# Performance work log

Measured on AMD Instinct MI355X. Metric: run time of the kernel, lower is better.

## Reference

```python
import jax, jax.numpy as jnp
import numpy as np

N, E, D, H, B = 10000, 160000, 128, 1, 4
SLOPE = 0.01  # negative_slope from DeepQNet default


def gat_layer(x, node_state, src, dst, W, att_src, att_dst, Wns, bns, bias):
    # x: [N,D] or [B,N,D]; node_state: [B,N,1]
    xs = x + node_state @ Wns + bns              # [B,N,D]
    Bx, Nn = xs.shape[0], xs.shape[1]
    h = (xs @ W).reshape(Bx, Nn, H, D)           # [B,N,H,C]
    a_src = (h * att_src).sum(-1)                # [B,N,H]
    a_dst = (h * att_dst).sum(-1)                # [B,N,H]
    ae = a_src[:, src] + a_dst[:, dst]           # [B,Etot,H]
    ae = jnp.where(ae > 0, ae, SLOPE * ae)       # leaky_relu
    ae_t = jnp.moveaxis(ae, 1, 0)                # [Etot,B,H]
    m = jax.ops.segment_max(ae_t, dst, num_segments=Nn)   # [N,B,H]
    e = jnp.exp(ae_t - m[dst])
    s = jax.ops.segment_sum(e, dst, num_segments=Nn)
    alpha = e / s[dst]                           # [Etot,B,H]
    h_e = jnp.moveaxis(h, 1, 0)                  # [N,B,H,C]
    msg = alpha[..., None] * h_e[src]            # [Etot,B,H,C]
    out = jax.ops.segment_sum(msg, dst, num_segments=Nn)  # [N,B,H,C]
    out = jnp.moveaxis(out, 0, 1).mean(2) + bias # concat=False -> head mean
    return jax.nn.relu(out)


def setup_inputs() -> dict:
    key = jax.random.key(0)
    ks = jax.random.split(key, 16)
    edges = jax.random.randint(ks[0], (2, E), 0, N)
    loop = jnp.arange(N)
    edge_index = jnp.concatenate([edges, jnp.stack([loop, loop])], axis=1)  # add_self_loops
    state = jax.random.uniform(ks[1], (B, N), dtype=jnp.float32)
    strucEmb = jax.random.normal(ks[2], (N, D), dtype=jnp.float32) * 0.1
    s = 0.05
    return {
        "state": state,
        "strucEmb": strucEmb,
        "edge_index": edge_index,
        "gat_W": jax.random.normal(ks[3], (3, D, H * D), dtype=jnp.float32) * s,
        "gat_att_src": jax.random.normal(ks[4], (3, H, D), dtype=jnp.float32) * s,
        "gat_att_dst": jax.random.normal(ks[5], (3, H, D), dtype=jnp.float32) * s,
        "gat_Wns": jax.random.normal(ks[6], (3, 1, D), dtype=jnp.float32) * s,
        "gat_bns": jnp.zeros((3, D), jnp.float32),
        "gat_bias": jnp.zeros((3, D), jnp.float32),
        "W1": jax.random.normal(ks[7], (D, D), dtype=jnp.float32) * s,
        "b1": jnp.zeros((D,), jnp.float32),
        "W2": jax.random.normal(ks[8], (D, D), dtype=jnp.float32) * s,
        "b2": jnp.zeros((D,), jnp.float32),
        "W3": jax.random.normal(ks[9], (2 * D, 1), dtype=jnp.float32) * s,
        "b3": jnp.zeros((1,), jnp.float32),
    }


def reference(state, strucEmb, edge_index, gat_W, gat_att_src, gat_att_dst,
              gat_Wns, gat_bns, gat_bias, W1, b1, W2, b2, W3, b3):
    src, dst = edge_index[0], edge_index[1]
    rs = state.reshape(state.shape[0], N, 1)     # [B,N,1]
    x = strucEmb
    for l in range(3):
        x = gat_layer(x, rs, src, dst, gat_W[l], gat_att_src[l], gat_att_dst[l],
                      gat_Wns[l], gat_bns[l], gat_bias[l])
    state_emb = x.sum(1)                         # [B,D]
    beta_state = state_emb @ W1 + b1             # [B,D]
    beta_action = x @ W2 + b2                    # [B,N,D]  (is_for_learn=True path)
    expand_state = jnp.broadcast_to(beta_state[:, None, :], beta_action.shape)
    out = jax.nn.relu(jnp.concatenate([expand_state, beta_action], axis=2))
    return out @ W3 + b3                         # [B,N,1]
```

## Files before the change

kernel.cpp:

```cpp
#include <hip/hip_runtime.h>
#include <math.h>

#define N_NODES 10000
#define B_SZ 4
#define SLOPE 0.01f
#define BN (B_SZ * N_NODES)
#define PADK 136

typedef __attribute__((ext_vector_type(8))) short short8;
typedef __attribute__((ext_vector_type(4))) short short4v;
typedef __attribute__((ext_vector_type(4))) float float4v;

__device__ __forceinline__ unsigned short f2bf(float f) {
    unsigned u = __builtin_bit_cast(unsigned, f);
    u += 0x7fffu + ((u >> 16) & 1u);
    return (unsigned short)(u >> 16);
}
__device__ __forceinline__ float bf2f(unsigned short s) {
    unsigned u = ((unsigned)s) << 16;
    return __builtin_bit_cast(float, u);
}


__global__ __launch_bounds__(256) void init_kernel(int* deg, int* cursor, float* state_emb) {
    int i = blockIdx.x * 256 + threadIdx.x;
    if (i < N_NODES) { deg[i] = 0; cursor[i] = 0; }
    if (i < B_SZ * 128) state_emb[i] = 0.f;
}

__global__ __launch_bounds__(256) void hist_kernel(const int* __restrict__ dst, int Etot, int* deg) {
    int e = blockIdx.x * 256 + threadIdx.x;
    if (e < Etot) atomicAdd(&deg[dst[e]], 1);
}

__global__ __launch_bounds__(1024) void scan_kernel(const int* __restrict__ deg, int* __restrict__ rowOff) {
    __shared__ int wsum[16];
    int tid = threadIdx.x;
    int lane = tid & 63, wid = tid >> 6;
    int base = tid * 10;
    int v[10]; int tot = 0;
#pragma unroll
    for (int j = 0; j < 10; j++) {
        int idx = base + j;
        int d = (idx < N_NODES) ? deg[idx] : 0;
        tot += d; v[j] = tot;
    }
    int incl = tot;
    for (int off = 1; off < 64; off <<= 1) {
        int t = __shfl_up(incl, off, 64);
        if (lane >= off) incl += t;
    }
    if (lane == 63) wsum[wid] = incl;
    __syncthreads();
    if (wid == 0) {
        int wv = (lane < 16) ? wsum[lane] : 0;
        for (int off = 1; off < 16; off <<= 1) {
            int t = __shfl_up(wv, off, 64);
            if (lane >= off) wv += t;
        }
        if (lane < 16) wsum[lane] = wv;
    }
    __syncthreads();
    int waveoff = (wid > 0) ? wsum[wid - 1] : 0;
    int excl = waveoff + incl - tot;
    if (tid == 0) rowOff[0] = 0;
#pragma unroll
    for (int j = 0; j < 10; j++) {
        int idx = base + j;
        if (idx < N_NODES) rowOff[idx + 1] = excl + v[j];
    }
}

__global__ __launch_bounds__(256) void scatter_kernel(const int* __restrict__ dst, int Etot,
                                                      const int* __restrict__ rowOff,
                                                      int* cursor, int* __restrict__ edgeLst) {
    int e = blockIdx.x * 256 + threadIdx.x;
    if (e < Etot) {
        int d = dst[e];
        int pos = rowOff[d] + atomicAdd(&cursor[d], 1);
        edgeLst[pos] = e;
    }
}


__global__ __launch_bounds__(256) void wconv_kernel(const float* __restrict__ gatW,
                                                    const float* __restrict__ W2,
                                                    unsigned short* __restrict__ whi,
                                                    unsigned short* __restrict__ wlo) {
    int w = blockIdx.y;
    int i = blockIdx.x * 256 + threadIdx.x;
    int k = i >> 7, c = i & 127;
    const float* src = (w < 3) ? (gatW + (size_t)w * 16384) : W2;
    float v = src[k * 128 + c];
    unsigned short h = f2bf(v);
    whi[w * 16384 + c * 128 + k] = h;
    wlo[w * 16384 + c * 128 + k] = f2bf(v - bf2f(h));
}


__global__ __launch_bounds__(256) void gemm_att_mfma(
    const float* __restrict__ xin, int layer0,
    const float* __restrict__ state,
    const unsigned short* __restrict__ WThi, const unsigned short* __restrict__ WTlo,
    const float* __restrict__ attS, const float* __restrict__ attD,
    const float* __restrict__ Wns, const float* __restrict__ bns,
    unsigned short* __restrict__ Hout, float* __restrict__ aSrcP, float* __restrict__ aDstP)
{
    __shared__ __align__(16) char smem[64 * PADK * 2 * 2];
    unsigned short* sAh = (unsigned short*)smem;
    unsigned short* sAl = sAh + 64 * PADK;
    unsigned short* sCus = (unsigned short*)smem;
    __shared__ float sWns[128], sBns[128], sAs[128], sAd[128];
    __shared__ float sPart[64 * 4 * 2];

    int tid = threadIdx.x;
    int g0 = blockIdx.x * 64;
    int w = tid >> 6, lane = tid & 63;
    int quad = lane >> 4, mcol = lane & 15;

    if (tid < 128) {
        sWns[tid] = Wns[tid]; sBns[tid] = bns[tid];
        sAs[tid] = attS[tid]; sAd[tid] = attD[tid];
    }

    short8 Bh[4][2], Bl[4][2];
#pragma unroll
    for (int kc = 0; kc < 4; kc++)
#pragma unroll
        for (int nt = 0; nt < 2; nt++) {
            int col = w * 32 + nt * 16 + mcol;
            Bh[kc][nt] = *(const short8*)(WThi + col * 128 + kc * 32 + quad * 8);
            Bl[kc][nt] = *(const short8*)(WTlo + col * 128 + kc * 32 + quad * 8);
        }

    __syncthreads();

    for (int i4 = tid; i4 < 64 * 32; i4 += 256) {
        int r = i4 >> 5, k4 = (i4 & 31) << 2;
        int g = g0 + r, n = g >> 2, b = g & 3;
        const float* src = layer0 ? (xin + (size_t)n * 128 + k4) : (xin + (size_t)g * 128 + k4);
        float4 v = *(const float4*)src;
        float st = state[b * N_NODES + n];
        float x0 = v.x + st * sWns[k4]     + sBns[k4];
        float x1 = v.y + st * sWns[k4 + 1] + sBns[k4 + 1];
        float x2 = v.z + st * sWns[k4 + 2] + sBns[k4 + 2];
        float x3 = v.w + st * sWns[k4 + 3] + sBns[k4 + 3];
        unsigned short h0 = f2bf(x0), h1 = f2bf(x1), h2 = f2bf(x2), h3 = f2bf(x3);
        short4v hv = { (short)h0, (short)h1, (short)h2, (short)h3 };
        short4v lv = { (short)f2bf(x0 - bf2f(h0)), (short)f2bf(x1 - bf2f(h1)),
                       (short)f2bf(x2 - bf2f(h2)), (short)f2bf(x3 - bf2f(h3)) };
        *(short4v*)(sAh + r * PADK + k4) = hv;
        *(short4v*)(sAl + r * PADK + k4) = lv;
    }
    __syncthreads();

    float4v acc[4][2];
#pragma unroll
    for (int mt = 0; mt < 4; mt++)
#pragma unroll
        for (int nt = 0; nt < 2; nt++) acc[mt][nt] = (float4v){0.f, 0.f, 0.f, 0.f};

#pragma unroll
    for (int kc = 0; kc < 4; kc++) {
#pragma unroll
        for (int mt = 0; mt < 4; mt++) {
            short8 ah = *(const short8*)(sAh + (mt * 16 + mcol) * PADK + kc * 32 + quad * 8);
            short8 al = *(const short8*)(sAl + (mt * 16 + mcol) * PADK + kc * 32 + quad * 8);
#pragma unroll
            for (int nt = 0; nt < 2; nt++) {
                acc[mt][nt] = __builtin_amdgcn_mfma_f32_16x16x32_bf16(ah, Bh[kc][nt], acc[mt][nt], 0, 0, 0);
                acc[mt][nt] = __builtin_amdgcn_mfma_f32_16x16x32_bf16(al, Bh[kc][nt], acc[mt][nt], 0, 0, 0);
                acc[mt][nt] = __builtin_amdgcn_mfma_f32_16x16x32_bf16(ah, Bl[kc][nt], acc[mt][nt], 0, 0, 0);
            }
        }
    }

    __syncthreads();

    float pp[16], pd[16];
#pragma unroll
    for (int r16 = 0; r16 < 16; r16++) { pp[r16] = 0.f; pd[r16] = 0.f; }
#pragma unroll
    for (int mt = 0; mt < 4; mt++)
#pragma unroll
        for (int nt = 0; nt < 2; nt++)
#pragma unroll
            for (int reg = 0; reg < 4; reg++) {
                int row = mt * 16 + quad * 4 + reg;
                int col = w * 32 + nt * 16 + mcol;
                float v = acc[mt][nt][reg];
                sCus[row * PADK + col] = f2bf(v);
                pp[mt * 4 + reg] += v * sAs[col];
                pd[mt * 4 + reg] += v * sAd[col];
            }
#pragma unroll
    for (int off = 1; off < 16; off <<= 1)
#pragma unroll
        for (int r16 = 0; r16 < 16; r16++) {
            pp[r16] += __shfl_xor(pp[r16], off);
            pd[r16] += __shfl_xor(pd[r16], off);
        }
    if (mcol == 0) {
#pragma unroll
        for (int r16 = 0; r16 < 16; r16++) {
            int row = (r16 >> 2) * 16 + quad * 4 + (r16 & 3);
            sPart[row * 8 + w * 2 + 0] = pp[r16];
            sPart[row * 8 + w * 2 + 1] = pd[r16];
        }
    }
    __syncthreads();

    for (int i = tid; i < 64 * 16; i += 256) {
        int r = i >> 4, c8 = i & 15;
        uint4 u = *(uint4*)(sCus + r * PADK + c8 * 8);
        *(uint4*)(Hout + (size_t)(g0 + r) * 128 + c8 * 8) = u;
    }
    if (tid < 64) {
        float s0 = sPart[tid * 8] + sPart[tid * 8 + 2] + sPart[tid * 8 + 4] + sPart[tid * 8 + 6];
        float s1 = sPart[tid * 8 + 1] + sPart[tid * 8 + 3] + sPart[tid * 8 + 5] + sPart[tid * 8 + 7];
        aSrcP[g0 + tid] = s0;
        aDstP[g0 + tid] = s1;
    }
}


__global__ __launch_bounds__(256) void sm_agg_kernel(
    const int* __restrict__ rowOff, const int* __restrict__ edgeLst,
    const int* __restrict__ srcArr,
    const float* __restrict__ aSrcP, const float* __restrict__ aDstP,
    const unsigned short* __restrict__ H,
    const float* __restrict__ bias, float* __restrict__ Xout)
{
    __shared__ int sSrc[64];
    __shared__ float sAl[64 * 4];
    int n = blockIdx.x;
    int start = rowOff[n], end = rowOff[n + 1];
    int tid = threadIdx.x;
    int b = tid >> 6, t = tid & 63;
    float adst = aDstP[n * 4 + b];

    float m = -1e30f;
    for (int i = start + t; i < end; i += 64) {
        int sn = srcArr[edgeLst[i]];
        float v = aSrcP[sn * 4 + b] + adst;
        m = fmaxf(m, v > 0.f ? v : SLOPE * v);
    }
    m = fmaxf(m, __shfl_xor(m, 1));  m = fmaxf(m, __shfl_xor(m, 2));
    m = fmaxf(m, __shfl_xor(m, 4));  m = fmaxf(m, __shfl_xor(m, 8));
    m = fmaxf(m, __shfl_xor(m, 16)); m = fmaxf(m, __shfl_xor(m, 32));

    float s = 0.f;
    for (int i = start + t; i < end; i += 64) {
        int sn = srcArr[edgeLst[i]];
        float v = aSrcP[sn * 4 + b] + adst;
        float ae = v > 0.f ? v : SLOPE * v;
        s += __expf(ae - m);
    }
    s += __shfl_xor(s, 1);  s += __shfl_xor(s, 2);  s += __shfl_xor(s, 4);
    s += __shfl_xor(s, 8);  s += __shfl_xor(s, 16); s += __shfl_xor(s, 32);
    float inv = 1.f / s;

    float accx = 0.f, accy = 0.f;
    const unsigned int* Hu = (const unsigned int*)H;
    for (int c0 = start; c0 < end; c0 += 64) {
        int cnt = min(64, end - c0);
        if (t < cnt) {
            int e = edgeLst[c0 + t];
            int sn = srcArr[e];
            if (b == 0) sSrc[t] = sn;
            float v = aSrcP[sn * 4 + b] + adst;
            float ae = v > 0.f ? v : SLOPE * v;
            sAl[t * 4 + b] = __expf(ae - m) * inv;
        }
        __syncthreads();
        int j = 0;
        for (; j + 4 <= cnt; j += 4) {
            int s0 = sSrc[j], s1 = sSrc[j + 1], s2 = sSrc[j + 2], s3 = sSrc[j + 3];
            float a0 = sAl[j * 4 + b], a1 = sAl[(j + 1) * 4 + b];
            float a2 = sAl[(j + 2) * 4 + b], a3 = sAl[(j + 3) * 4 + b];
            unsigned int h0 = Hu[(size_t)(s0 * 4 + b) * 64 + t];
            unsigned int h1 = Hu[(size_t)(s1 * 4 + b) * 64 + t];
            unsigned int h2 = Hu[(size_t)(s2 * 4 + b) * 64 + t];
            unsigned int h3 = Hu[(size_t)(s3 * 4 + b) * 64 + t];
            accx += a0 * __builtin_bit_cast(float, h0 << 16) + a1 * __builtin_bit_cast(float, h1 << 16)
                  + a2 * __builtin_bit_cast(float, h2 << 16) + a3 * __builtin_bit_cast(float, h3 << 16);
            accy += a0 * __builtin_bit_cast(float, h0 & 0xffff0000u) + a1 * __builtin_bit_cast(float, h1 & 0xffff0000u)
                  + a2 * __builtin_bit_cast(float, h2 & 0xffff0000u) + a3 * __builtin_bit_cast(float, h3 & 0xffff0000u);
        }
        for (; j < cnt; j++) {
            int s0 = sSrc[j];
            float a0 = sAl[j * 4 + b];
            unsigned int h0 = Hu[(size_t)(s0 * 4 + b) * 64 + t];
            accx += a0 * __builtin_bit_cast(float, h0 << 16);
            accy += a0 * __builtin_bit_cast(float, h0 & 0xffff0000u);
        }
        __syncthreads();
    }
    float ox = accx + bias[2 * t];
    float oy = accy + bias[2 * t + 1];
    ((float2*)Xout)[(size_t)(n * 4 + b) * 64 + t] = make_float2(ox > 0.f ? ox : 0.f, oy > 0.f ? oy : 0.f);
}


__global__ __launch_bounds__(128) void sum_nodes_kernel(const float* __restrict__ X, float* state_emb) {
    int cx = blockIdx.x, b = blockIdx.y, d = threadIdx.x;
    int n0 = cx * 157, n1 = n0 + 157;
    if (n1 > N_NODES) n1 = N_NODES;
    float acc = 0.f;
    for (int n = n0; n < n1; n++) acc += X[(size_t)(n * 4 + b) * 128 + d];
    atomicAdd(&state_emb[b * 128 + d], acc);
}

__global__ __launch_bounds__(512) void beta_state_kernel(
    const float* __restrict__ state_emb, const float* __restrict__ W1,
    const float* __restrict__ b1, const float* __restrict__ W3, float* c1)
{
    __shared__ float sm[512];
    int tid = threadIdx.x;
    int b = tid >> 7, d = tid & 127;
    float acc = b1[d];
    for (int k = 0; k < 128; k++) acc += state_emb[b * 128 + k] * W1[k * 128 + d];
    float v = acc > 0.f ? acc : 0.f;
    sm[tid] = v * W3[d];
    __syncthreads();
    for (int s = 64; s > 0; s >>= 1) {
        if (d < s) sm[tid] += sm[tid + s];
        __syncthreads();
    }
    if (d == 0) c1[b] = sm[tid];
}


__global__ __launch_bounds__(256) void final_mfma(
    const float* __restrict__ X,
    const unsigned short* __restrict__ WThi, const unsigned short* __restrict__ WTlo,
    const float* __restrict__ b2, const float* __restrict__ W3,
    const float* __restrict__ b3, const float* __restrict__ c1,
    float* __restrict__ out)
{
    __shared__ __align__(16) char smem[64 * PADK * 2 * 2];
    unsigned short* sAh = (unsigned short*)smem;
    unsigned short* sAl = sAh + 64 * PADK;
    __shared__ float sB2[128], sW3[128];
    __shared__ float sPart[64 * 4];

    int tid = threadIdx.x;
    int g0 = blockIdx.x * 64;
    int w = tid >> 6, lane = tid & 63;
    int quad = lane >> 4, mcol = lane & 15;

    if (tid < 128) { sB2[tid] = b2[tid]; sW3[tid] = W3[128 + tid]; }

    short8 Bh[4][2], Bl[4][2];
#pragma unroll
    for (int kc = 0; kc < 4; kc++)
#pragma unroll
        for (int nt = 0; nt < 2; nt++) {
            int col = w * 32 + nt * 16 + mcol;
            Bh[kc][nt] = *(const short8*)(WThi + col * 128 + kc * 32 + quad * 8);
            Bl[kc][nt] = *(const short8*)(WTlo + col * 128 + kc * 32 + quad * 8);
        }

    for (int i4 = tid; i4 < 64 * 32; i4 += 256) {
        int r = i4 >> 5, k4 = (i4 & 31) << 2;
        int g = g0 + r;
        float4 v = *(const float4*)(X + (size_t)g * 128 + k4);
        unsigned short h0 = f2bf(v.x), h1 = f2bf(v.y), h2 = f2bf(v.z), h3 = f2bf(v.w);
        short4v hv = { (short)h0, (short)h1, (short)h2, (short)h3 };
        short4v lv = { (short)f2bf(v.x - bf2f(h0)), (short)f2bf(v.y - bf2f(h1)),
                       (short)f2bf(v.z - bf2f(h2)), (short)f2bf(v.w - bf2f(h3)) };
        *(short4v*)(sAh + r * PADK + k4) = hv;
        *(short4v*)(sAl + r * PADK + k4) = lv;
    }
    __syncthreads();

    float4v acc[4][2];
#pragma unroll
    for (int mt = 0; mt < 4; mt++)
#pragma unroll
        for (int nt = 0; nt < 2; nt++) acc[mt][nt] = (float4v){0.f, 0.f, 0.f, 0.f};

#pragma unroll
    for (int kc = 0; kc < 4; kc++) {
#pragma unroll
        for (int mt = 0; mt < 4; mt++) {
            short8 ah = *(const short8*)(sAh + (mt * 16 + mcol) * PADK + kc * 32 + quad * 8);
            short8 al = *(const short8*)(sAl + (mt * 16 + mcol) * PADK + kc * 32 + quad * 8);
#pragma unroll
            for (int nt = 0; nt < 2; nt++) {
                acc[mt][nt] = __builtin_amdgcn_mfma_f32_16x16x32_bf16(ah, Bh[kc][nt], acc[mt][nt], 0, 0, 0);
                acc[mt][nt] = __builtin_amdgcn_mfma_f32_16x16x32_bf16(al, Bh[kc][nt], acc[mt][nt], 0, 0, 0);
                acc[mt][nt] = __builtin_amdgcn_mfma_f32_16x16x32_bf16(ah, Bl[kc][nt], acc[mt][nt], 0, 0, 0);
            }
        }
    }

    float pp[16];
#pragma unroll
    for (int r16 = 0; r16 < 16; r16++) pp[r16] = 0.f;
#pragma unroll
    for (int mt = 0; mt < 4; mt++)
#pragma unroll
        for (int nt = 0; nt < 2; nt++)
#pragma unroll
            for (int reg = 0; reg < 4; reg++) {
                int col = w * 32 + nt * 16 + mcol;
                float v = acc[mt][nt][reg] + sB2[col];
                v = v > 0.f ? v : 0.f;
                pp[mt * 4 + reg] += v * sW3[col];
            }
#pragma unroll
    for (int off = 1; off < 16; off <<= 1)
#pragma unroll
        for (int r16 = 0; r16 < 16; r16++)
            pp[r16] += __shfl_xor(pp[r16], off);
    if (mcol == 0) {
#pragma unroll
        for (int r16 = 0; r16 < 16; r16++) {
            int row = (r16 >> 2) * 16 + quad * 4 + (r16 & 3);
            sPart[row * 4 + w] = pp[r16];
        }
    }
    __syncthreads();
    if (tid < 64) {
        float p = sPart[tid * 4] + sPart[tid * 4 + 1] + sPart[tid * 4 + 2] + sPart[tid * 4 + 3];
        int g = g0 + tid;
        out[(g & 3) * N_NODES + (g >> 2)] = p + c1[g & 3] + b3[0];
    }
}


extern "C" void kernel_launch(void* const* d_in, const int* in_sizes, int n_in,
                              void* d_out, int out_size, void* d_ws, size_t ws_size,
                              hipStream_t stream) {
    const float* state    = (const float*)d_in[0];
    const float* strucEmb = (const float*)d_in[1];
    const int*   edge_idx = (const int*)d_in[2];
    const float* gat_W    = (const float*)d_in[3];
    const float* gat_aS   = (const float*)d_in[4];
    const float* gat_aD   = (const float*)d_in[5];
    const float* gat_Wns  = (const float*)d_in[6];
    const float* gat_bns  = (const float*)d_in[7];
    const float* gat_bias = (const float*)d_in[8];
    const float* W1 = (const float*)d_in[9];
    const float* b1 = (const float*)d_in[10];
    const float* W2 = (const float*)d_in[11];
    const float* b2 = (const float*)d_in[12];
    const float* W3 = (const float*)d_in[13];
    const float* b3 = (const float*)d_in[14];
    float* out = (float*)d_out;

    int Etot = in_sizes[2] / 2;
    const int* srcArr = edge_idx;
    const int* dstArr = edge_idx + Etot;

    float* ws = (float*)d_ws;
    float* X           = ws;
    unsigned short* Hb = (unsigned short*)(ws + 5120000);
    float* aSrcP       = ws + 10240000;
    float* aDstP       = ws + 10280000;
    float* state_emb   = ws + 10320000;
    float* c1          = ws + 10320512;
    unsigned short* whi = (unsigned short*)(ws + 10320516);
    unsigned short* wlo = whi + 4 * 16384;
    int*   iws         = (int*)(ws + 10320516 + 65536);
    int*   rowOff      = iws;
    int*   deg         = iws + 10001;
    int*   cursor      = deg + 10000;
    int*   edgeLst     = cursor + 10000;

    wconv_kernel<<<dim3(64, 4), 256, 0, stream>>>(gat_W, W2, whi, wlo);
    init_kernel<<<40, 256, 0, stream>>>(deg, cursor, state_emb);
    hist_kernel<<<(Etot + 255) / 256, 256, 0, stream>>>(dstArr, Etot, deg);
    scan_kernel<<<1, 1024, 0, stream>>>(deg, rowOff);
    scatter_kernel<<<(Etot + 255) / 256, 256, 0, stream>>>(dstArr, Etot, rowOff, cursor, edgeLst);

    for (int l = 0; l < 3; l++) {
        gemm_att_mfma<<<BN / 64, 256, 0, stream>>>(
            l == 0 ? strucEmb : X, l == 0 ? 1 : 0, state,
            whi + (size_t)l * 16384, wlo + (size_t)l * 16384,
            gat_aS + l * 128, gat_aD + l * 128,
            gat_Wns + l * 128, gat_bns + l * 128, Hb, aSrcP, aDstP);
        sm_agg_kernel<<<N_NODES, 256, 0, stream>>>(
            rowOff, edgeLst, srcArr, aSrcP, aDstP, Hb, gat_bias + l * 128, X);
    }

    sum_nodes_kernel<<<dim3(64, B_SZ), 128, 0, stream>>>(X, state_emb);
    beta_state_kernel<<<1, 512, 0, stream>>>(state_emb, W1, b1, W3, c1);
    final_mfma<<<BN / 64, 256, 0, stream>>>(X, whi + 3 * 16384, wlo + 3 * 16384,
                                            b2, W3, b3, c1, out);
}
```

Measured before the change: 350.2 us.

## Store activations as bf16, fuse next-layer state add into aggregation, single-pass softmax

Activations between layers are now stored as single bf16 values instead of fp32. The next layer's node_state@Wns+bns term is fused into the aggregation epilogue, and a prep kernel builds the layer-0 input. The GEMMs load A fragments straight from global memory, which removes the shared-memory staging and drops the A-lo MFMA pass (two MFMAs instead of three). The aggregation kernel does a single-pass softmax for nodes with at most 64 edges, normalising at the end. This cuts memory traffic and redundant edge passes, at the cost of lower activation precision.

```diff
diff --git a/kernel.cpp b/kernel.cpp
--- a/kernel.cpp
+++ b/kernel.cpp
@@ -8,7 +8,6 @@
 #define PADK 136
 
 typedef __attribute__((ext_vector_type(8))) short short8;
-typedef __attribute__((ext_vector_type(4))) short short4v;
 typedef __attribute__((ext_vector_type(4))) float float4v;
 
 __device__ __forceinline__ unsigned short f2bf(float f) {
@@ -98,30 +97,35 @@
 }
 
 
+__global__ __launch_bounds__(256) void prep0_kernel(const float* __restrict__ strucEmb,
+                                                    const float* __restrict__ state,
+                                                    const float* __restrict__ Wns0,
+                                                    const float* __restrict__ bns0,
+                                                    unsigned short* __restrict__ XS) {
+    int idx = blockIdx.x * 256 + threadIdx.x;
+    int g = idx >> 7, d = idx & 127;
+    int n = g >> 2, b = g & 3;
+    float v = strucEmb[(size_t)n * 128 + d] + state[b * N_NODES + n] * Wns0[d] + bns0[d];
+    XS[idx] = f2bf(v);
+}
+
+
 __global__ __launch_bounds__(256) void gemm_att_mfma(
-    const float* __restrict__ xin, int layer0,
-    const float* __restrict__ state,
+    const unsigned short* __restrict__ XS,
     const unsigned short* __restrict__ WThi, const unsigned short* __restrict__ WTlo,
     const float* __restrict__ attS, const float* __restrict__ attD,
-    const float* __restrict__ Wns, const float* __restrict__ bns,
     unsigned short* __restrict__ Hout, float* __restrict__ aSrcP, float* __restrict__ aDstP)
 {
-    __shared__ __align__(16) char smem[64 * PADK * 2 * 2];
-    unsigned short* sAh = (unsigned short*)smem;
-    unsigned short* sAl = sAh + 64 * PADK;
-    unsigned short* sCus = (unsigned short*)smem;
-    __shared__ float sWns[128], sBns[128], sAs[128], sAd[128];
-    __shared__ float sPart[64 * 4 * 2];
+    __shared__ __align__(16) unsigned short sCus[64 * PADK];
+    __shared__ float sAs[128], sAd[128];
+    __shared__ float sPart[64 * 8];
 
     int tid = threadIdx.x;
     int g0 = blockIdx.x * 64;
     int w = tid >> 6, lane = tid & 63;
     int quad = lane >> 4, mcol = lane & 15;
 
-    if (tid < 128) {
-        sWns[tid] = Wns[tid]; sBns[tid] = bns[tid];
-        sAs[tid] = attS[tid]; sAd[tid] = attD[tid];
-    }
+    if (tid < 128) { sAs[tid] = attS[tid]; sAd[tid] = attD[tid]; }
 
     short8 Bh[4][2], Bl[4][2];
 #pragma unroll
@@ -132,27 +136,12 @@
             Bh[kc][nt] = *(const short8*)(WThi + col * 128 + kc * 32 + quad * 8);
             Bl[kc][nt] = *(const short8*)(WTlo + col * 128 + kc * 32 + quad * 8);
         }
-
-    __syncthreads();
-
-    for (int i4 = tid; i4 < 64 * 32; i4 += 256) {
-        int r = i4 >> 5, k4 = (i4 & 31) << 2;
-        int g = g0 + r, n = g >> 2, b = g & 3;
-        const float* src = layer0 ? (xin + (size_t)n * 128 + k4) : (xin + (size_t)g * 128 + k4);
-        float4 v = *(const float4*)src;
-        float st = state[b * N_NODES + n];
-        float x0 = v.x + st * sWns[k4]     + sBns[k4];
-        float x1 = v.y + st * sWns[k4 + 1] + sBns[k4 + 1];
-        float x2 = v.z + st * sWns[k4 + 2] + sBns[k4 + 2];
-        float x3 = v.w + st * sWns[k4 + 3] + sBns[k4 + 3];
-        unsigned short h0 = f2bf(x0), h1 = f2bf(x1), h2 = f2bf(x2), h3 = f2bf(x3);
-        short4v hv = { (short)h0, (short)h1, (short)h2, (short)h3 };
-        short4v lv = { (short)f2bf(x0 - bf2f(h0)), (short)f2bf(x1 - bf2f(h1)),
-                       (short)f2bf(x2 - bf2f(h2)), (short)f2bf(x3 - bf2f(h3)) };
-        *(short4v*)(sAh + r * PADK + k4) = hv;
-        *(short4v*)(sAl + r * PADK + k4) = lv;
-    }
-    __syncthreads();
+    short8 Af[4][4];
+#pragma unroll
+    for (int mt = 0; mt < 4; mt++)
+#pragma unroll
+        for (int kc = 0; kc < 4; kc++)
+            Af[mt][kc] = *(const short8*)(XS + (size_t)(g0 + mt * 16 + mcol) * 128 + kc * 32 + quad * 8);
 
     float4v acc[4][2];
 #pragma unroll
@@ -161,19 +150,14 @@
         for (int nt = 0; nt < 2; nt++) acc[mt][nt] = (float4v){0.f, 0.f, 0.f, 0.f};
 
 #pragma unroll
-    for (int kc = 0; kc < 4; kc++) {
-#pragma unroll
-        for (int mt = 0; mt < 4; mt++) {
-            short8 ah = *(const short8*)(sAh + (mt * 16 + mcol) * PADK + kc * 32 + quad * 8);
-            short8 al = *(const short8*)(sAl + (mt * 16 + mcol) * PADK + kc * 32 + quad * 8);
+    for (int kc = 0; kc < 4; kc++)
+#pragma unroll
+        for (int mt = 0; mt < 4; mt++)
 #pragma unroll
             for (int nt = 0; nt < 2; nt++) {
-                acc[mt][nt] = __builtin_amdgcn_mfma_f32_16x16x32_bf16(ah, Bh[kc][nt], acc[mt][nt], 0, 0, 0);
-                acc[mt][nt] = __builtin_amdgcn_mfma_f32_16x16x32_bf16(al, Bh[kc][nt], acc[mt][nt], 0, 0, 0);
-                acc[mt][nt] = __builtin_amdgcn_mfma_f32_16x16x32_bf16(ah, Bl[kc][nt], acc[mt][nt], 0, 0, 0);
+                acc[mt][nt] = __builtin_amdgcn_mfma_f32_16x16x32_bf16(Af[mt][kc], Bh[kc][nt], acc[mt][nt], 0, 0, 0);
+                acc[mt][nt] = __builtin_amdgcn_mfma_f32_16x16x32_bf16(Af[mt][kc], Bl[kc][nt], acc[mt][nt], 0, 0, 0);
             }
-        }
-    }
 
     __syncthreads();
 
@@ -229,55 +213,45 @@
     const int* __restrict__ srcArr,
     const float* __restrict__ aSrcP, const float* __restrict__ aDstP,
     const unsigned short* __restrict__ H,
-    const float* __restrict__ bias, float* __restrict__ Xout)
+    const float* __restrict__ bias,
+    const float* __restrict__ state, const float* __restrict__ wnsN,
+    const float* __restrict__ bnsN, int addNext,
+    unsigned short* __restrict__ Xout)
 {
     __shared__ int sSrc[64];
-    __shared__ float sAl[64 * 4];
+    __shared__ float sAe[64 * 4];
     int n = blockIdx.x;
     int start = rowOff[n], end = rowOff[n + 1];
+    int cnt = end - start;
     int tid = threadIdx.x;
     int b = tid >> 6, t = tid & 63;
     float adst = aDstP[n * 4 + b];
-
-    float m = -1e30f;
-    for (int i = start + t; i < end; i += 64) {
-        int sn = srcArr[edgeLst[i]];
-        float v = aSrcP[sn * 4 + b] + adst;
-        m = fmaxf(m, v > 0.f ? v : SLOPE * v);
-    }
-    m = fmaxf(m, __shfl_xor(m, 1));  m = fmaxf(m, __shfl_xor(m, 2));
-    m = fmaxf(m, __shfl_xor(m, 4));  m = fmaxf(m, __shfl_xor(m, 8));
-    m = fmaxf(m, __shfl_xor(m, 16)); m = fmaxf(m, __shfl_xor(m, 32));
-
-    float s = 0.f;
-    for (int i = start + t; i < end; i += 64) {
-        int sn = srcArr[edgeLst[i]];
-        float v = aSrcP[sn * 4 + b] + adst;
-        float ae = v > 0.f ? v : SLOPE * v;
-        s += __expf(ae - m);
-    }
-    s += __shfl_xor(s, 1);  s += __shfl_xor(s, 2);  s += __shfl_xor(s, 4);
-    s += __shfl_xor(s, 8);  s += __shfl_xor(s, 16); s += __shfl_xor(s, 32);
-    float inv = 1.f / s;
-
-    float accx = 0.f, accy = 0.f;
     const unsigned int* Hu = (const unsigned int*)H;
-    for (int c0 = start; c0 < end; c0 += 64) {
-        int cnt = min(64, end - c0);
+
+    float accx = 0.f, accy = 0.f, inv = 0.f;
+
+    if (cnt <= 64) {
+        float ae = -1e30f;
         if (t < cnt) {
-            int e = edgeLst[c0 + t];
+            int e = edgeLst[start + t];
             int sn = srcArr[e];
             if (b == 0) sSrc[t] = sn;
             float v = aSrcP[sn * 4 + b] + adst;
-            float ae = v > 0.f ? v : SLOPE * v;
-            sAl[t * 4 + b] = __expf(ae - m) * inv;
-        }
+            ae = v > 0.f ? v : SLOPE * v;
+            sAe[t * 4 + b] = ae;
+        }
+        float m = ae;
+        m = fmaxf(m, __shfl_xor(m, 1));  m = fmaxf(m, __shfl_xor(m, 2));
+        m = fmaxf(m, __shfl_xor(m, 4));  m = fmaxf(m, __shfl_xor(m, 8));
+        m = fmaxf(m, __shfl_xor(m, 16)); m = fmaxf(m, __shfl_xor(m, 32));
         __syncthreads();
+        float s = 0.f;
         int j = 0;
         for (; j + 4 <= cnt; j += 4) {
+            float a0 = __expf(sAe[j * 4 + b] - m),       a1 = __expf(sAe[(j + 1) * 4 + b] - m);
+            float a2 = __expf(sAe[(j + 2) * 4 + b] - m), a3 = __expf(sAe[(j + 3) * 4 + b] - m);
             int s0 = sSrc[j], s1 = sSrc[j + 1], s2 = sSrc[j + 2], s3 = sSrc[j + 3];
-            float a0 = sAl[j * 4 + b], a1 = sAl[(j + 1) * 4 + b];
-            float a2 = sAl[(j + 2) * 4 + b], a3 = sAl[(j + 3) * 4 + b];
+            s += a0 + a1 + a2 + a3;
             unsigned int h0 = Hu[(size_t)(s0 * 4 + b) * 64 + t];
             unsigned int h1 = Hu[(size_t)(s1 * 4 + b) * 64 + t];
             unsigned int h2 = Hu[(size_t)(s2 * 4 + b) * 64 + t];
@@ -288,26 +262,76 @@
                   + a2 * __builtin_bit_cast(float, h2 & 0xffff0000u) + a3 * __builtin_bit_cast(float, h3 & 0xffff0000u);
         }
         for (; j < cnt; j++) {
+            float a0 = __expf(sAe[j * 4 + b] - m);
             int s0 = sSrc[j];
-            float a0 = sAl[j * 4 + b];
+            s += a0;
             unsigned int h0 = Hu[(size_t)(s0 * 4 + b) * 64 + t];
             accx += a0 * __builtin_bit_cast(float, h0 << 16);
             accy += a0 * __builtin_bit_cast(float, h0 & 0xffff0000u);
         }
-        __syncthreads();
-    }
-    float ox = accx + bias[2 * t];
-    float oy = accy + bias[2 * t + 1];
-    ((float2*)Xout)[(size_t)(n * 4 + b) * 64 + t] = make_float2(ox > 0.f ? ox : 0.f, oy > 0.f ? oy : 0.f);
-}
-
-
-__global__ __launch_bounds__(128) void sum_nodes_kernel(const float* __restrict__ X, float* state_emb) {
+        inv = 1.f / s;
+    } else {
+        float m = -1e30f;
+        for (int i = start + t; i < end; i += 64) {
+            int sn = srcArr[edgeLst[i]];
+            float v = aSrcP[sn * 4 + b] + adst;
+            m = fmaxf(m, v > 0.f ? v : SLOPE * v);
+        }
+        m = fmaxf(m, __shfl_xor(m, 1));  m = fmaxf(m, __shfl_xor(m, 2));
+        m = fmaxf(m, __shfl_xor(m, 4));  m = fmaxf(m, __shfl_xor(m, 8));
+        m = fmaxf(m, __shfl_xor(m, 16)); m = fmaxf(m, __shfl_xor(m, 32));
+        float s = 0.f;
+        for (int i = start + t; i < end; i += 64) {
+            int sn = srcArr[edgeLst[i]];
+            float v = aSrcP[sn * 4 + b] + adst;
+            float ae = v > 0.f ? v : SLOPE * v;
+            s += __expf(ae - m);
+        }
+        s += __shfl_xor(s, 1);  s += __shfl_xor(s, 2);  s += __shfl_xor(s, 4);
+        s += __shfl_xor(s, 8);  s += __shfl_xor(s, 16); s += __shfl_xor(s, 32);
+        for (int c0 = start; c0 < end; c0 += 64) {
+            int c = min(64, end - c0);
+            if (t < c) {
+                int e = edgeLst[c0 + t];
+                int sn = srcArr[e];
+                if (b == 0) sSrc[t] = sn;
+                float v = aSrcP[sn * 4 + b] + adst;
+                float ae = v > 0.f ? v : SLOPE * v;
+                sAe[t * 4 + b] = __expf(ae - m);
+            }
+            __syncthreads();
+            for (int j = 0; j < c; j++) {
+                float a0 = sAe[j * 4 + b];
+                int s0 = sSrc[j];
+                unsigned int h0 = Hu[(size_t)(s0 * 4 + b) * 64 + t];
+                accx += a0 * __builtin_bit_cast(float, h0 << 16);
+                accy += a0 * __builtin_bit_cast(float, h0 & 0xffff0000u);
+            }
+            __syncthreads();
+        }
+        inv = 1.f / s;
+    }
+
+    float ox = accx * inv + bias[2 * t];
+    float oy = accy * inv + bias[2 * t + 1];
+    ox = ox > 0.f ? ox : 0.f;
+    oy = oy > 0.f ? oy : 0.f;
+    if (addNext) {
+        float st = state[b * N_NODES + n];
+        ox += st * wnsN[2 * t]     + bnsN[2 * t];
+        oy += st * wnsN[2 * t + 1] + bnsN[2 * t + 1];
+    }
+    unsigned px = f2bf(ox), py = f2bf(oy);
+    ((unsigned*)Xout)[(size_t)(n * 4 + b) * 64 + t] = (py << 16) | px;
+}
+
+
+__global__ __launch_bounds__(128) void sum_nodes_kernel(const unsigned short* __restrict__ X, float* state_emb) {
     int cx = blockIdx.x, b = blockIdx.y, d = threadIdx.x;
     int n0 = cx * 157, n1 = n0 + 157;
     if (n1 > N_NODES) n1 = N_NODES;
     float acc = 0.f;
-    for (int n = n0; n < n1; n++) acc += X[(size_t)(n * 4 + b) * 128 + d];
+    for (int n = n0; n < n1; n++) acc += bf2f(X[(size_t)(n * 4 + b) * 128 + d]);
     atomicAdd(&state_emb[b * 128 + d], acc);
 }
 
@@ -332,15 +356,12 @@
 
 
 __global__ __launch_bounds__(256) void final_mfma(
-    const float* __restrict__ X,
+    const unsigned short* __restrict__ X,
     const unsigned short* __restrict__ WThi, const unsigned short* __restrict__ WTlo,
     const float* __restrict__ b2, const float* __restrict__ W3,
     const float* __restrict__ b3, const float* __restrict__ c1,
     float* __restrict__ out)
 {
-    __shared__ __align__(16) char smem[64 * PADK * 2 * 2];
-    unsigned short* sAh = (unsigned short*)smem;
-    unsigned short* sAl = sAh + 64 * PADK;
     __shared__ float sB2[128], sW3[128];
     __shared__ float sPart[64 * 4];
 
@@ -360,19 +381,12 @@
             Bh[kc][nt] = *(const short8*)(WThi + col * 128 + kc * 32 + quad * 8);
             Bl[kc][nt] = *(const short8*)(WTlo + col * 128 + kc * 32 + quad * 8);
         }
-
-    for (int i4 = tid; i4 < 64 * 32; i4 += 256) {
-        int r = i4 >> 5, k4 = (i4 & 31) << 2;
-        int g = g0 + r;
-        float4 v = *(const float4*)(X + (size_t)g * 128 + k4);
-        unsigned short h0 = f2bf(v.x), h1 = f2bf(v.y), h2 = f2bf(v.z), h3 = f2bf(v.w);
-        short4v hv = { (short)h0, (short)h1, (short)h2, (short)h3 };
-        short4v lv = { (short)f2bf(v.x - bf2f(h0)), (short)f2bf(v.y - bf2f(h1)),
-                       (short)f2bf(v.z - bf2f(h2)), (short)f2bf(v.w - bf2f(h3)) };
-        *(short4v*)(sAh + r * PADK + k4) = hv;
-        *(short4v*)(sAl + r * PADK + k4) = lv;
-    }
-    __syncthreads();
+    short8 Af[4][4];
+#pragma unroll
+    for (int mt = 0; mt < 4; mt++)
+#pragma unroll
+        for (int kc = 0; kc < 4; kc++)
+            Af[mt][kc] = *(const short8*)(X + (size_t)(g0 + mt * 16 + mcol) * 128 + kc * 32 + quad * 8);
 
     float4v acc[4][2];
 #pragma unroll
@@ -381,19 +395,16 @@
         for (int nt = 0; nt < 2; nt++) acc[mt][nt] = (float4v){0.f, 0.f, 0.f, 0.f};
 
 #pragma unroll
-    for (int kc = 0; kc < 4; kc++) {
-#pragma unroll
-        for (int mt = 0; mt < 4; mt++) {
-            short8 ah = *(const short8*)(sAh + (mt * 16 + mcol) * PADK + kc * 32 + quad * 8);
-            short8 al = *(const short8*)(sAl + (mt * 16 + mcol) * PADK + kc * 32 + quad * 8);
+    for (int kc = 0; kc < 4; kc++)
+#pragma unroll
+        for (int mt = 0; mt < 4; mt++)
 #pragma unroll
             for (int nt = 0; nt < 2; nt++) {
-                acc[mt][nt] = __builtin_amdgcn_mfma_f32_16x16x32_bf16(ah, Bh[kc][nt], acc[mt][nt], 0, 0, 0);
-                acc[mt][nt] = __builtin_amdgcn_mfma_f32_16x16x32_bf16(al, Bh[kc][nt], acc[mt][nt], 0, 0, 0);
-                acc[mt][nt] = __builtin_amdgcn_mfma_f32_16x16x32_bf16(ah, Bl[kc][nt], acc[mt][nt], 0, 0, 0);
+                acc[mt][nt] = __builtin_amdgcn_mfma_f32_16x16x32_bf16(Af[mt][kc], Bh[kc][nt], acc[mt][nt], 0, 0, 0);
+                acc[mt][nt] = __builtin_amdgcn_mfma_f32_16x16x32_bf16(Af[mt][kc], Bl[kc][nt], acc[mt][nt], 0, 0, 0);
             }
-        }
-    }
+
+    __syncthreads();
 
     float pp[16];
 #pragma unroll
@@ -455,15 +466,15 @@
     const int* dstArr = edge_idx + Etot;
 
     float* ws = (float*)d_ws;
-    float* X           = ws;
-    unsigned short* Hb = (unsigned short*)(ws + 5120000);
-    float* aSrcP       = ws + 10240000;
-    float* aDstP       = ws + 10280000;
-    float* state_emb   = ws + 10320000;
-    float* c1          = ws + 10320512;
-    unsigned short* whi = (unsigned short*)(ws + 10320516);
+    unsigned short* Xb = (unsigned short*)ws;
+    unsigned short* Hb = (unsigned short*)(ws + 2560000);
+    float* aSrcP       = ws + 5120000;
+    float* aDstP       = ws + 5160000;
+    float* state_emb   = ws + 5200000;
+    float* c1          = ws + 5200512;
+    unsigned short* whi = (unsigned short*)(ws + 5200516);
     unsigned short* wlo = whi + 4 * 16384;
-    int*   iws         = (int*)(ws + 10320516 + 65536);
+    int*   iws         = (int*)(ws + 5200516 + 65536);
     int*   rowOff      = iws;
     int*   deg         = iws + 10001;
     int*   cursor      = deg + 10000;
@@ -471,22 +482,23 @@
 
     wconv_kernel<<<dim3(64, 4), 256, 0, stream>>>(gat_W, W2, whi, wlo);
     init_kernel<<<40, 256, 0, stream>>>(deg, cursor, state_emb);
+    prep0_kernel<<<BN * 128 / 256, 256, 0, stream>>>(strucEmb, state, gat_Wns, gat_bns, Xb);
     hist_kernel<<<(Etot + 255) / 256, 256, 0, stream>>>(dstArr, Etot, deg);
     scan_kernel<<<1, 1024, 0, stream>>>(deg, rowOff);
     scatter_kernel<<<(Etot + 255) / 256, 256, 0, stream>>>(dstArr, Etot, rowOff, cursor, edgeLst);
 
     for (int l = 0; l < 3; l++) {
         gemm_att_mfma<<<BN / 64, 256, 0, stream>>>(
-            l == 0 ? strucEmb : X, l == 0 ? 1 : 0, state,
-            whi + (size_t)l * 16384, wlo + (size_t)l * 16384,
-            gat_aS + l * 128, gat_aD + l * 128,
-            gat_Wns + l * 128, gat_bns + l * 128, Hb, aSrcP, aDstP);
+            Xb, whi + (size_t)l * 16384, wlo + (size_t)l * 16384,
+            gat_aS + l * 128, gat_aD + l * 128, Hb, aSrcP, aDstP);
         sm_agg_kernel<<<N_NODES, 256, 0, stream>>>(
-            rowOff, edgeLst, srcArr, aSrcP, aDstP, Hb, gat_bias + l * 128, X);
-    }
-
-    sum_nodes_kernel<<<dim3(64, B_SZ), 128, 0, stream>>>(X, state_emb);
+            rowOff, edgeLst, srcArr, aSrcP, aDstP, Hb, gat_bias + l * 128,
+            state, gat_Wns + (l + 1 < 3 ? (l + 1) * 128 : 0),
+            gat_bns + (l + 1 < 3 ? (l + 1) * 128 : 0), (l < 2) ? 1 : 0, Xb);
+    }
+
+    sum_nodes_kernel<<<dim3(64, B_SZ), 128, 0, stream>>>(Xb, state_emb);
     beta_state_kernel<<<1, 512, 0, stream>>>(state_emb, W1, b1, W3, c1);
-    final_mfma<<<BN / 64, 256, 0, stream>>>(X, whi + 3 * 16384, wlo + 3 * 16384,
+    final_mfma<<<BN / 64, 256, 0, stream>>>(Xb, whi + 3 * 16384, wlo + 3 * 16384,
                                             b2, W3, b3, c1, out);
 }
```

New measurement: 339.8 us. -3.0%, faster.
